# Optimization experiments

Measured on AMD Instinct MI355X. Metric: run time of the kernel, lower is better.

## Reference

```python
import jax, jax.numpy as jnp
import numpy as np

H = 1024      # hidden_size
NH = 16       # num_heads
HD = H // NH  # head_dim
E = 4096      # expand_size
EPS = 1e-5


def layernorm(x, w, b):
    mu = jnp.mean(x, axis=-1, keepdims=True)
    var = jnp.mean(jnp.square(x - mu), axis=-1, keepdims=True)
    return (x - mu) * jax.lax.rsqrt(var + EPS) * w + b


def setup_inputs() -> dict:
    key = jax.random.key(0)
    ks = jax.random.split(key, 8)
    s = 1.0 / np.sqrt(H)
    return {
        "x": jax.random.normal(ks[0], (4, 2048, H), dtype=jnp.float32),
        "ln1_w": jnp.ones((H,), jnp.float32),
        "ln1_b": jnp.zeros((H,), jnp.float32),
        "Wqkv": jax.random.normal(ks[1], (H, 3 * H), dtype=jnp.float32) * s,
        "bqkv": jnp.zeros((3 * H,), jnp.float32),
        "Wo": jax.random.normal(ks[2], (H, H), dtype=jnp.float32) * s,
        "bo": jnp.zeros((H,), jnp.float32),
        "ln2_w": jnp.ones((H,), jnp.float32),
        "ln2_b": jnp.zeros((H,), jnp.float32),
        "fc1_w": jax.random.normal(ks[3], (H, E), dtype=jnp.float32) * s,
        "fc1_b": jnp.zeros((E,), jnp.float32),
        "fc2_w": jax.random.normal(ks[4], (E, H), dtype=jnp.float32) * (1.0 / np.sqrt(E)),
        "fc2_b": jnp.zeros((H,), jnp.float32),
    }


def reference(x, ln1_w, ln1_b, Wqkv, bqkv, Wo, bo, ln2_w, ln2_b, fc1_w, fc1_b, fc2_w, fc2_b):
    B, S, C = x.shape
    # --- attention sub-block (pre-norm) ---
    h = layernorm(x, ln1_w, ln1_b)
    qkv = h @ Wqkv + bqkv                             # [B,S,3C]
    qkv = qkv.reshape(B, S, 3, NH, HD)
    q, k, v = (jnp.moveaxis(qkv[:, :, i], 2, 1) for i in range(3))  # [B,NH,S,HD]
    attn = jnp.einsum("bhqd,bhkd->bhqk", q, k) / np.sqrt(HD)        # [B,NH,S,S]
    attn = jax.nn.softmax(attn, axis=-1)
    o = jnp.einsum("bhqk,bhkd->bhqd", attn, v)        # [B,NH,S,HD]
    o = jnp.moveaxis(o, 1, 2).reshape(B, S, C)
    x = x + o @ Wo + bo
    # --- FFN sub-block (pre-norm) ---
    h = layernorm(x, ln2_w, ln2_b)
    h = jax.nn.gelu(h @ fc1_w + fc1_b, approximate=False)
    return x + h @ fc2_w + fc2_b
```

## Files before the change

### kernel.cpp

```cpp
#include <hip/hip_runtime.h>
#include <hip/hip_bf16.h>
#include <math.h>

typedef __bf16 bf16_t;
typedef __bf16 bf16x4 __attribute__((ext_vector_type(4)));
typedef short  s16x8  __attribute__((ext_vector_type(8)));
typedef float  f32x4  __attribute__((ext_vector_type(4)));

#define DEVINL __device__ __forceinline__

DEVINL void gload_lds16(const void* g, void* l) {
  __builtin_amdgcn_global_load_lds(
      (const __attribute__((address_space(1))) unsigned int*)g,
      (__attribute__((address_space(3))) unsigned int*)l, 16, 0, 0);
}

DEVINL f32x4 mfma16(s16x8 a, s16x8 b, f32x4 c) {
  return __builtin_amdgcn_mfma_f32_16x16x32_bf16(a, b, c, 0, 0, 0);
}

__global__ __launch_bounds__(256) void tcast_kernel(const float* __restrict__ W,
                                                    bf16_t* __restrict__ WT,
                                                    int K, int N) {
  __shared__ float tile[32][33];
  const int n0 = blockIdx.x * 32, k0 = blockIdx.y * 32;
  const int tx = threadIdx.x, ty = threadIdx.y;
#pragma unroll
  for (int j = 0; j < 4; ++j)
    tile[ty + j * 8][tx] = W[(size_t)(k0 + ty + j * 8) * N + (n0 + tx)];
  __syncthreads();
#pragma unroll
  for (int j = 0; j < 4; ++j)
    WT[(size_t)(n0 + ty + j * 8) * K + (k0 + tx)] = (bf16_t)tile[tx][ty + j * 8];
}

__global__ __launch_bounds__(256) void ln_kernel(const float* __restrict__ x,
                                                 const float* __restrict__ w,
                                                 const float* __restrict__ b,
                                                 bf16_t* __restrict__ out) {
  const int row = blockIdx.x, tid = threadIdx.x;
  const float4 v = ((const float4*)(x + (size_t)row * 1024))[tid];
  float s  = v.x + v.y + v.z + v.w;
  float s2 = v.x * v.x + v.y * v.y + v.z * v.z + v.w * v.w;
#pragma unroll
  for (int off = 32; off > 0; off >>= 1) {
    s  += __shfl_down(s, off);
    s2 += __shfl_down(s2, off);
  }
  __shared__ float red[8];
  const int wave = tid >> 6, lane = tid & 63;
  if (lane == 0) { red[wave] = s; red[4 + wave] = s2; }
  __syncthreads();
  s  = red[0] + red[1] + red[2] + red[3];
  s2 = red[4] + red[5] + red[6] + red[7];
  const float mu = s * (1.0f / 1024.0f);
  const float rs = rsqrtf(s2 * (1.0f / 1024.0f) - mu * mu + 1e-5f);
  const float4 wv = ((const float4*)w)[tid];
  const float4 bv = ((const float4*)b)[tid];
  bf16x4 o;
  o[0] = (bf16_t)((v.x - mu) * rs * wv.x + bv.x);
  o[1] = (bf16_t)((v.y - mu) * rs * wv.y + bv.y);
  o[2] = (bf16_t)((v.z - mu) * rs * wv.z + bv.z);
  o[3] = (bf16_t)((v.w - mu) * rs * wv.w + bv.w);
  ((bf16x4*)(out + (size_t)row * 1024))[tid] = o;
}

template <int EPI>
__global__ __launch_bounds__(256, 4) void gemm128b(const bf16_t* __restrict__ A,
                                                   const bf16_t* __restrict__ BT,
                                                   const float* __restrict__ bias,
                                                   const float* __restrict__ resid,
                                                   void* __restrict__ out,
                                                   void* __restrict__ out2,
                                                   int M, int N, int K) {
  __shared__ __align__(16) bf16_t sA[128 * 64];
  __shared__ __align__(16) bf16_t sB[128 * 64];
  const int tid = threadIdx.x;
  const int lane = tid & 63, wave = tid >> 6;
  const int wr = wave >> 1, wc = wave & 1;
  const int g = lane >> 4, lr = lane & 15;

  const int bid = blockIdx.x;
  const int cpx = gridDim.x >> 3;
  const int gid = (bid & 7) * cpx + (bid >> 3);
  const int m0 = (gid & 63) * 128, n0 = (gid >> 6) * 128;
  const bf16_t* Ab = A + (size_t)m0 * K;
  const bf16_t* Bb = BT + (size_t)n0 * K;

  f32x4 acc[4][4] = {};

  for (int kt = 0; kt < K; kt += 64) {
    __syncthreads();
#pragma unroll
    for (int q = 0; q < 4; ++q) {
      const int c = q * 256 + tid;
      const int r = c >> 3;
      const int j = (c & 7) ^ (r & 7);
      const size_t doff = (size_t)(q * 256 + wave * 64) * 8;
      gload_lds16(Ab + (size_t)r * K + kt + j * 8, sA + doff);
      gload_lds16(Bb + (size_t)r * K + kt + j * 8, sB + doff);
    }
    __syncthreads();
#pragma unroll
    for (int ks = 0; ks < 2; ++ks) {
      s16x8 af[4], bfr[4];
#pragma unroll
      for (int m = 0; m < 4; ++m) {
        const int r = wr * 64 + m * 16 + lr;
        af[m] = *(const s16x8*)&sA[r * 64 + (((ks << 2) + g) ^ (r & 7)) * 8];
      }
#pragma unroll
      for (int n = 0; n < 4; ++n) {
        const int r = wc * 64 + n * 16 + lr;
        bfr[n] = *(const s16x8*)&sB[r * 64 + (((ks << 2) + g) ^ (r & 7)) * 8];
      }
#pragma unroll
      for (int m = 0; m < 4; ++m)
#pragma unroll
        for (int n = 0; n < 4; ++n)
          acc[m][n] = mfma16(af[m], bfr[n], acc[m][n]);
    }
  }

#pragma unroll
  for (int m = 0; m < 4; ++m)
#pragma unroll
    for (int n = 0; n < 4; ++n) {
      const int col = n0 + wc * 64 + n * 16 + lr;
      const float bv = bias[col];
      const int rrow0 = m0 + wr * 64 + m * 16 + g * 4;
      if (EPI == 3 && col >= 2048) {
        const int col2 = col - 2048;
        bf16x4 pk;
#pragma unroll
        for (int i = 0; i < 4; ++i) pk[i] = (bf16_t)(acc[m][n][i] + bv);
        const size_t didx =
            ((((size_t)(rrow0 >> 11)) * 16 + (col2 >> 6)) * 64 + (col2 & 63)) * 2048 +
            (rrow0 & 2047);
        *(bf16x4*)&((bf16_t*)out2)[didx] = pk;
      } else {
#pragma unroll
        for (int i = 0; i < 4; ++i) {
          const int rrow = rrow0 + i;
          float v = acc[m][n][i] + bv;
          if (EPI == 1) {
            const size_t idx = (size_t)rrow * N + col;
            v += resid[idx];
            ((float*)out)[idx] = v;
          } else if (EPI == 2) {
            v = 0.5f * v * (1.0f + erff(v * 0.70710678118f));
            ((bf16_t*)out)[(size_t)rrow * N + col] = (bf16_t)v;
          } else if (EPI == 3) {
            ((bf16_t*)out)[(size_t)rrow * 2048 + col] = (bf16_t)v;
          } else {
            ((bf16_t*)out)[(size_t)rrow * N + col] = (bf16_t)v;
          }
        }
      }
    }
}

__global__ __launch_bounds__(256) void flash_attn2(const bf16_t* __restrict__ qk,
                                                   const bf16_t* __restrict__ vt,
                                                   bf16_t* __restrict__ O) {
  const int S = 2048;
  const int qt = blockIdx.x;
  const int bh = blockIdx.y;
  const int h = bh & 15;
  const size_t rowbase = (size_t)(bh >> 4) * S;
  const int tid = threadIdx.x, lane = tid & 63, wave = tid >> 6;
  const int g = lane >> 4, lr = lane & 15;
  const int q0w = qt * 64 + wave * 16;

  __shared__ __align__(16) bf16_t sK[64 * 64];
  __shared__ __align__(16) bf16_t sVT[64 * 64];
  __shared__ __align__(16) bf16_t sP[4][16 * 72];

  const bf16_t* vtb = vt + (size_t)bh * 64 * 2048;

  s16x8 aq[2];
  {
    const bf16_t* qrow = qk + (rowbase + q0w + lr) * 2048 + h * 64;
    aq[0] = *(const s16x8*)(qrow + g * 8);
    aq[1] = *(const s16x8*)(qrow + 32 + g * 8);
  }

  f32x4 oa[4] = {};
  float mrun = -1e30f, lrun = 0.0f;

  for (int kv0 = 0; kv0 < S; kv0 += 64) {
    __syncthreads();
#pragma unroll
    for (int p = 0; p < 2; ++p) {
      const int c = p * 256 + wave * 64 + lane;
      const int r = c >> 3;
      const int pb = (c & 7) ^ (r & 7);
      char* dK = (char*)sK + (size_t)(p * 256 + wave * 64) * 16;
      char* dV = (char*)sVT + (size_t)(p * 256 + wave * 64) * 16;
      gload_lds16(qk + (rowbase + kv0 + r) * 2048 + 1024 + h * 64 + pb * 8, dK);
      gload_lds16(vtb + (size_t)r * 2048 + kv0 + pb * 8, dV);
    }
    __syncthreads();

    f32x4 sc[4] = {};
#pragma unroll
    for (int st = 0; st < 2; ++st)
#pragma unroll
      for (int fr = 0; fr < 4; ++fr) {
        const int pb = (g + 4 * st) ^ (lr & 7);
        const s16x8 ak = *(const s16x8*)&sK[(fr * 16 + lr) * 64 + pb * 8];
        sc[fr] = mfma16(ak, aq[st], sc[fr]);
      }

    float rmax = -1e30f;
#pragma unroll
    for (int fr = 0; fr < 4; ++fr)
#pragma unroll
      for (int i = 0; i < 4; ++i) rmax = fmaxf(rmax, sc[fr][i]);
    rmax = fmaxf(rmax, __shfl_xor(rmax, 16));
    rmax = fmaxf(rmax, __shfl_xor(rmax, 32));
    const float mnew = fmaxf(mrun, rmax * 0.125f);
    const float alpha = __expf(mrun - mnew);
    mrun = mnew;
    float rsum = 0.0f;
#pragma unroll
    for (int fr = 0; fr < 4; ++fr)
#pragma unroll
      for (int i = 0; i < 4; ++i) {
        const float pp = __expf(sc[fr][i] * 0.125f - mnew);
        sc[fr][i] = pp;
        rsum += pp;
      }
    rsum += __shfl_xor(rsum, 16);
    rsum += __shfl_xor(rsum, 32);
    lrun = lrun * alpha + rsum;
#pragma unroll
    for (int f2 = 0; f2 < 4; ++f2)
#pragma unroll
      for (int i = 0; i < 4; ++i) oa[f2][i] *= alpha;

#pragma unroll
    for (int fr = 0; fr < 4; ++fr) {
      bf16x4 pk;
#pragma unroll
      for (int i = 0; i < 4; ++i) pk[i] = (bf16_t)sc[fr][i];
      *(bf16x4*)&sP[wave][lr * 72 + fr * 16 + 4 * g] = pk;
    }

#pragma unroll
    for (int st = 0; st < 2; ++st) {
      const s16x8 pa = *(const s16x8*)&sP[wave][lr * 72 + st * 32 + g * 8];
#pragma unroll
      for (int f2 = 0; f2 < 4; ++f2) {
        const int pb = (g + 4 * st) ^ (lr & 7);
        const s16x8 va = *(const s16x8*)&sVT[(f2 * 16 + lr) * 64 + pb * 8];
        oa[f2] = mfma16(va, pa, oa[f2]);
      }
    }
  }

  const float rl = 1.0f / lrun;
#pragma unroll
  for (int f2 = 0; f2 < 4; ++f2) {
    bf16x4 ov;
#pragma unroll
    for (int i = 0; i < 4; ++i) ov[i] = (bf16_t)(oa[f2][i] * rl);
    *(bf16x4*)&O[(rowbase + q0w + lr) * 1024 + h * 64 + f2 * 16 + 4 * g] = ov;
  }
}

extern "C" void kernel_launch(void* const* d_in, const int* in_sizes, int n_in,
                              void* d_out, int out_size, void* d_ws, size_t ws_size,
                              hipStream_t stream) {
  const float* x    = (const float*)d_in[0];
  const float* ln1w = (const float*)d_in[1];
  const float* ln1b = (const float*)d_in[2];
  const float* Wqkv = (const float*)d_in[3];
  const float* bqkv = (const float*)d_in[4];
  const float* Wo   = (const float*)d_in[5];
  const float* bo   = (const float*)d_in[6];
  const float* ln2w = (const float*)d_in[7];
  const float* ln2b = (const float*)d_in[8];
  const float* fc1w = (const float*)d_in[9];
  const float* fc1b = (const float*)d_in[10];
  const float* fc2w = (const float*)d_in[11];
  const float* fc2b = (const float*)d_in[12];

  const int M = 8192;

  char* ws = (char*)d_ws;
  size_t off = 0;
  auto alloc = [&](size_t bytes) {
    char* p = ws + off;
    off += (bytes + 255) & ~(size_t)255;
    return p;
  };
  bf16_t* WqkvT = (bf16_t*)alloc((size_t)3072 * 1024 * 2);
  bf16_t* WoT   = (bf16_t*)alloc((size_t)1024 * 1024 * 2);
  bf16_t* fc1T  = (bf16_t*)alloc((size_t)4096 * 1024 * 2);
  bf16_t* fc2T  = (bf16_t*)alloc((size_t)1024 * 4096 * 2);
  bf16_t* h1    = (bf16_t*)alloc((size_t)M * 1024 * 2);
  bf16_t* qkQK  = (bf16_t*)alloc((size_t)M * 2048 * 2);
  bf16_t* vTg   = (bf16_t*)alloc((size_t)M * 1024 * 2);
  bf16_t* attnO = (bf16_t*)alloc((size_t)M * 1024 * 2);
  float*  x2    = (float*)alloc((size_t)M * 1024 * 4);
  bf16_t* h2   = h1;
  bf16_t* gbuf = qkQK;
  if (off > ws_size) return;

  const dim3 tb(32, 8);
  tcast_kernel<<<dim3(96, 32), tb, 0, stream>>>(Wqkv, WqkvT, 1024, 3072);
  tcast_kernel<<<dim3(32, 32), tb, 0, stream>>>(Wo, WoT, 1024, 1024);
  tcast_kernel<<<dim3(128, 32), tb, 0, stream>>>(fc1w, fc1T, 1024, 4096);
  tcast_kernel<<<dim3(32, 128), tb, 0, stream>>>(fc2w, fc2T, 4096, 1024);

  ln_kernel<<<M, 256, 0, stream>>>(x, ln1w, ln1b, h1);

  gemm128b<3><<<dim3(1536), 256, 0, stream>>>(h1, WqkvT, bqkv, nullptr, qkQK, vTg, M, 3072, 1024);

  flash_attn2<<<dim3(32, 64), 256, 0, stream>>>(qkQK, vTg, attnO);

  gemm128b<1><<<dim3(512), 256, 0, stream>>>(attnO, WoT, bo, x, x2, nullptr, M, 1024, 1024);

  ln_kernel<<<M, 256, 0, stream>>>(x2, ln2w, ln2b, h2);

  gemm128b<2><<<dim3(2048), 256, 0, stream>>>(h2, fc1T, fc1b, nullptr, gbuf, nullptr, M, 4096, 1024);

  gemm128b<1><<<dim3(512), 256, 0, stream>>>(gbuf, fc2T, fc2b, x2, (float*)d_out, nullptr, M, 1024, 4096);
}
```

Measured before the change: 449.0 us.

## Process 32 query rows per wave in flash attention with lazy rescaling

Each wave now handles two 16-row query tiles (128 queries per block, half the blocks), so every K/V tile loaded into LDS is reused across twice as many queries. The softmax moves to exp2 with a folded scale constant and skips the running-max rescale unless the new max exceeds the old by more than 8 (log2 units). The P staging buffer uses an XOR-style rotated layout without padding, and s_setprio brackets the MFMA sections. The cost is more registers per thread and fewer blocks in flight, which may lower occupancy.

Result: slower. 471.6 us (+5.0%).

```diff
diff --git a/kernel.cpp b/kernel.cpp
--- a/kernel.cpp
+++ b/kernel.cpp
@@ -160,7 +160,7 @@
     }
 }
 
-__global__ __launch_bounds__(256) void flash_attn2(const bf16_t* __restrict__ qk,
+__global__ __launch_bounds__(256) void flash_attn3(const bf16_t* __restrict__ qk,
                                                    const bf16_t* __restrict__ vt,
                                                    bf16_t* __restrict__ O) {
   const int S = 2048;
@@ -170,23 +170,26 @@
   const size_t rowbase = (size_t)(bh >> 4) * S;
   const int tid = threadIdx.x, lane = tid & 63, wave = tid >> 6;
   const int g = lane >> 4, lr = lane & 15;
-  const int q0w = qt * 64 + wave * 16;
+  const int q0w = qt * 128 + wave * 32;
+  const float c2 = 0.18033688f;
 
   __shared__ __align__(16) bf16_t sK[64 * 64];
   __shared__ __align__(16) bf16_t sVT[64 * 64];
-  __shared__ __align__(16) bf16_t sP[4][16 * 72];
+  __shared__ __align__(16) bf16_t sP[4][16 * 64];
 
   const bf16_t* vtb = vt + (size_t)bh * 64 * 2048;
 
-  s16x8 aq[2];
-  {
-    const bf16_t* qrow = qk + (rowbase + q0w + lr) * 2048 + h * 64;
-    aq[0] = *(const s16x8*)(qrow + g * 8);
-    aq[1] = *(const s16x8*)(qrow + 32 + g * 8);
-  }
-
-  f32x4 oa[4] = {};
-  float mrun = -1e30f, lrun = 0.0f;
+  s16x8 aq[2][2];
+#pragma unroll
+  for (int hf = 0; hf < 2; ++hf) {
+    const bf16_t* qrow = qk + (rowbase + q0w + hf * 16 + lr) * 2048 + h * 64;
+    aq[hf][0] = *(const s16x8*)(qrow + g * 8);
+    aq[hf][1] = *(const s16x8*)(qrow + 32 + g * 8);
+  }
+
+  f32x4 oa[2][4] = {};
+  float m2[2] = {-1e30f, -1e30f};
+  float lrun[2] = {0.0f, 0.0f};
 
   for (int kv0 = 0; kv0 < S; kv0 += 64) {
     __syncthreads();
@@ -202,70 +205,87 @@
     }
     __syncthreads();
 
-    f32x4 sc[4] = {};
-#pragma unroll
-    for (int st = 0; st < 2; ++st)
+#pragma unroll
+    for (int hf = 0; hf < 2; ++hf) {
+      f32x4 sc[4] = {};
+      __builtin_amdgcn_s_setprio(1);
+#pragma unroll
+      for (int st = 0; st < 2; ++st)
+#pragma unroll
+        for (int fr = 0; fr < 4; ++fr) {
+          const int pb = (g + 4 * st) ^ (lr & 7);
+          const s16x8 ak = *(const s16x8*)&sK[(fr * 16 + lr) * 64 + pb * 8];
+          sc[fr] = mfma16(ak, aq[hf][st], sc[fr]);
+        }
+      __builtin_amdgcn_s_setprio(0);
+
+      float rmax = fmaxf(fmaxf(sc[0][0], sc[0][1]), fmaxf(sc[0][2], sc[0][3]));
+#pragma unroll
+      for (int fr = 1; fr < 4; ++fr)
+#pragma unroll
+        for (int i = 0; i < 4; ++i) rmax = fmaxf(rmax, sc[fr][i]);
+      rmax = fmaxf(rmax, __shfl_xor(rmax, 16));
+      rmax = fmaxf(rmax, __shfl_xor(rmax, 32));
+      const float pm2 = rmax * c2;
+      if (!__all(pm2 <= m2[hf] + 8.0f)) {
+        const float mn = fmaxf(m2[hf], pm2);
+        const float alpha = exp2f(m2[hf] - mn);
+        m2[hf] = mn;
+        lrun[hf] *= alpha;
+#pragma unroll
+        for (int f2 = 0; f2 < 4; ++f2)
+#pragma unroll
+          for (int i = 0; i < 4; ++i) oa[hf][f2][i] *= alpha;
+      }
+      const float mm = m2[hf];
+      float rsum = 0.0f;
+#pragma unroll
+      for (int fr = 0; fr < 4; ++fr)
+#pragma unroll
+        for (int i = 0; i < 4; ++i) {
+          const float pp = exp2f(fmaf(sc[fr][i], c2, -mm));
+          sc[fr][i] = pp;
+          rsum += pp;
+        }
+      rsum += __shfl_xor(rsum, 16);
+      rsum += __shfl_xor(rsum, 32);
+      lrun[hf] += rsum;
+
 #pragma unroll
       for (int fr = 0; fr < 4; ++fr) {
-        const int pb = (g + 4 * st) ^ (lr & 7);
-        const s16x8 ak = *(const s16x8*)&sK[(fr * 16 + lr) * 64 + pb * 8];
-        sc[fr] = mfma16(ak, aq[st], sc[fr]);
-      }
-
-    float rmax = -1e30f;
-#pragma unroll
-    for (int fr = 0; fr < 4; ++fr)
-#pragma unroll
-      for (int i = 0; i < 4; ++i) rmax = fmaxf(rmax, sc[fr][i]);
-    rmax = fmaxf(rmax, __shfl_xor(rmax, 16));
-    rmax = fmaxf(rmax, __shfl_xor(rmax, 32));
-    const float mnew = fmaxf(mrun, rmax * 0.125f);
-    const float alpha = __expf(mrun - mnew);
-    mrun = mnew;
-    float rsum = 0.0f;
-#pragma unroll
-    for (int fr = 0; fr < 4; ++fr)
-#pragma unroll
-      for (int i = 0; i < 4; ++i) {
-        const float pp = __expf(sc[fr][i] * 0.125f - mnew);
-        sc[fr][i] = pp;
-        rsum += pp;
-      }
-    rsum += __shfl_xor(rsum, 16);
-    rsum += __shfl_xor(rsum, 32);
-    lrun = lrun * alpha + rsum;
-#pragma unroll
-    for (int f2 = 0; f2 < 4; ++f2)
-#pragma unroll
-      for (int i = 0; i < 4; ++i) oa[f2][i] *= alpha;
-
-#pragma unroll
-    for (int fr = 0; fr < 4; ++fr) {
-      bf16x4 pk;
-#pragma unroll
-      for (int i = 0; i < 4; ++i) pk[i] = (bf16_t)sc[fr][i];
-      *(bf16x4*)&sP[wave][lr * 72 + fr * 16 + 4 * g] = pk;
-    }
-
-#pragma unroll
-    for (int st = 0; st < 2; ++st) {
-      const s16x8 pa = *(const s16x8*)&sP[wave][lr * 72 + st * 32 + g * 8];
-#pragma unroll
-      for (int f2 = 0; f2 < 4; ++f2) {
-        const int pb = (g + 4 * st) ^ (lr & 7);
-        const s16x8 va = *(const s16x8*)&sVT[(f2 * 16 + lr) * 64 + pb * 8];
-        oa[f2] = mfma16(va, pa, oa[f2]);
-      }
-    }
-  }
-
-  const float rl = 1.0f / lrun;
-#pragma unroll
-  for (int f2 = 0; f2 < 4; ++f2) {
-    bf16x4 ov;
-#pragma unroll
-    for (int i = 0; i < 4; ++i) ov[i] = (bf16_t)(oa[f2][i] * rl);
-    *(bf16x4*)&O[(rowbase + q0w + lr) * 1024 + h * 64 + f2 * 16 + 4 * g] = ov;
+        bf16x4 pk;
+#pragma unroll
+        for (int i = 0; i < 4; ++i) pk[i] = (bf16_t)sc[fr][i];
+        const int c = fr * 2 + (g >> 1);
+        *(bf16x4*)&sP[wave][lr * 64 + ((c + lr) & 7) * 8 + 4 * (g & 1)] = pk;
+      }
+
+      __builtin_amdgcn_s_setprio(1);
+#pragma unroll
+      for (int st = 0; st < 2; ++st) {
+        const int pc = st * 4 + g;
+        const s16x8 pa = *(const s16x8*)&sP[wave][lr * 64 + ((pc + lr) & 7) * 8];
+#pragma unroll
+        for (int f2 = 0; f2 < 4; ++f2) {
+          const int pb = (g + 4 * st) ^ (lr & 7);
+          const s16x8 va = *(const s16x8*)&sVT[(f2 * 16 + lr) * 64 + pb * 8];
+          oa[hf][f2] = mfma16(va, pa, oa[hf][f2]);
+        }
+      }
+      __builtin_amdgcn_s_setprio(0);
+    }
+  }
+
+#pragma unroll
+  for (int hf = 0; hf < 2; ++hf) {
+    const float rl = 1.0f / lrun[hf];
+#pragma unroll
+    for (int f2 = 0; f2 < 4; ++f2) {
+      bf16x4 ov;
+#pragma unroll
+      for (int i = 0; i < 4; ++i) ov[i] = (bf16_t)(oa[hf][f2][i] * rl);
+      *(bf16x4*)&O[(rowbase + q0w + hf * 16 + lr) * 1024 + h * 64 + f2 * 16 + 4 * g] = ov;
+    }
   }
 }
 
@@ -318,7 +338,7 @@
 
   gemm128b<3><<<dim3(1536), 256, 0, stream>>>(h1, WqkvT, bqkv, nullptr, qkQK, vTg, M, 3072, 1024);
 
-  flash_attn2<<<dim3(32, 64), 256, 0, stream>>>(qkQK, vTg, attnO);
+  flash_attn3<<<dim3(16, 64), 256, 0, stream>>>(qkQK, vTg, attnO);
 
   gemm128b<1><<<dim3(512), 256, 0, stream>>>(attnO, WoT, bo, x, x2, nullptr, M, 1024, 1024);
 
```

## Double-buffer K/V tiles and add lazy rescaling with exp2 in flash attention

Applied to the files above, without the earlier changes.

The attention kernel now double-buffers the K and V^T tiles in LDS, so the next tile is issued into the other buffer while the current one is computed, and each iteration needs one barrier instead of two. Softmax uses exp2 with a pre-folded log2e/sqrt(d) scale, and the output/denominator rescale is skipped unless some row's max grows by more than 8 in log2 space. The P scratch buffer drops its padding in favour of an XOR-like rotated layout, and s_setprio is raised around the MFMA sections. In exchange it doubles K/V LDS use, which may lower occupancy. The lazy rescale lets exponentials reach up to 2^8 before renormalisation, which shifts bf16 rounding of P slightly.

Result: slower. 463.4 us (+3.2%).

```diff
diff --git a/kernel.cpp b/kernel.cpp
--- a/kernel.cpp
+++ b/kernel.cpp
@@ -160,7 +160,7 @@
     }
 }
 
-__global__ __launch_bounds__(256) void flash_attn2(const bf16_t* __restrict__ qk,
+__global__ __launch_bounds__(256) void flash_attn4(const bf16_t* __restrict__ qk,
                                                    const bf16_t* __restrict__ vt,
                                                    bf16_t* __restrict__ O) {
   const int S = 2048;
@@ -171,12 +171,34 @@
   const int tid = threadIdx.x, lane = tid & 63, wave = tid >> 6;
   const int g = lane >> 4, lr = lane & 15;
   const int q0w = qt * 64 + wave * 16;
-
-  __shared__ __align__(16) bf16_t sK[64 * 64];
-  __shared__ __align__(16) bf16_t sVT[64 * 64];
-  __shared__ __align__(16) bf16_t sP[4][16 * 72];
+  const float c2 = 0.18033688f;
+
+  __shared__ __align__(16) bf16_t sK[2][64 * 64];
+  __shared__ __align__(16) bf16_t sVT[2][64 * 64];
+  __shared__ __align__(16) bf16_t sP[4][16 * 64];
 
   const bf16_t* vtb = vt + (size_t)bh * 64 * 2048;
+
+  const bf16_t* kp[2];
+  const bf16_t* vp[2];
+  int ldsoff[2];
+#pragma unroll
+  for (int p = 0; p < 2; ++p) {
+    const int cp = p * 256 + wave * 64 + lane;
+    const int r = cp >> 3;
+    const int pb = (cp & 7) ^ (r & 7);
+    kp[p] = qk + (rowbase + r) * 2048 + 1024 + h * 64 + pb * 8;
+    vp[p] = vtb + (size_t)r * 2048 + pb * 8;
+    ldsoff[p] = (p * 256 + wave * 64) * 16;
+  }
+  auto stage = [&](int t, int buf) {
+    const int kvoff = t << 6;
+#pragma unroll
+    for (int p = 0; p < 2; ++p) {
+      gload_lds16(kp[p] + (size_t)kvoff * 2048, (char*)sK[buf] + ldsoff[p]);
+      gload_lds16(vp[p] + kvoff, (char*)sVT[buf] + ldsoff[p]);
+    }
+  };
 
   s16x8 aq[2];
   {
@@ -186,77 +208,80 @@
   }
 
   f32x4 oa[4] = {};
-  float mrun = -1e30f, lrun = 0.0f;
-
-  for (int kv0 = 0; kv0 < S; kv0 += 64) {
+  float m2 = -1e30f, lrun = 0.0f;
+
+  stage(0, 0);
+
+  for (int t = 0; t < 32; ++t) {
+    const int cur = t & 1;
     __syncthreads();
-#pragma unroll
-    for (int p = 0; p < 2; ++p) {
-      const int c = p * 256 + wave * 64 + lane;
-      const int r = c >> 3;
-      const int pb = (c & 7) ^ (r & 7);
-      char* dK = (char*)sK + (size_t)(p * 256 + wave * 64) * 16;
-      char* dV = (char*)sVT + (size_t)(p * 256 + wave * 64) * 16;
-      gload_lds16(qk + (rowbase + kv0 + r) * 2048 + 1024 + h * 64 + pb * 8, dK);
-      gload_lds16(vtb + (size_t)r * 2048 + kv0 + pb * 8, dV);
-    }
-    __syncthreads();
+    if (t + 1 < 32) stage(t + 1, cur ^ 1);
 
     f32x4 sc[4] = {};
+    __builtin_amdgcn_s_setprio(1);
 #pragma unroll
     for (int st = 0; st < 2; ++st)
 #pragma unroll
       for (int fr = 0; fr < 4; ++fr) {
         const int pb = (g + 4 * st) ^ (lr & 7);
-        const s16x8 ak = *(const s16x8*)&sK[(fr * 16 + lr) * 64 + pb * 8];
+        const s16x8 ak = *(const s16x8*)&sK[cur][(fr * 16 + lr) * 64 + pb * 8];
         sc[fr] = mfma16(ak, aq[st], sc[fr]);
       }
-
-    float rmax = -1e30f;
-#pragma unroll
-    for (int fr = 0; fr < 4; ++fr)
+    __builtin_amdgcn_s_setprio(0);
+
+    float rmax = fmaxf(fmaxf(sc[0][0], sc[0][1]), fmaxf(sc[0][2], sc[0][3]));
+#pragma unroll
+    for (int fr = 1; fr < 4; ++fr)
 #pragma unroll
       for (int i = 0; i < 4; ++i) rmax = fmaxf(rmax, sc[fr][i]);
     rmax = fmaxf(rmax, __shfl_xor(rmax, 16));
     rmax = fmaxf(rmax, __shfl_xor(rmax, 32));
-    const float mnew = fmaxf(mrun, rmax * 0.125f);
-    const float alpha = __expf(mrun - mnew);
-    mrun = mnew;
+    const float pm2 = rmax * c2;
+    if (!__all(pm2 <= m2 + 8.0f)) {
+      const float mn = fmaxf(m2, pm2);
+      const float alpha = exp2f(m2 - mn);
+      m2 = mn;
+      lrun *= alpha;
+#pragma unroll
+      for (int f2 = 0; f2 < 4; ++f2)
+#pragma unroll
+        for (int i = 0; i < 4; ++i) oa[f2][i] *= alpha;
+    }
     float rsum = 0.0f;
 #pragma unroll
     for (int fr = 0; fr < 4; ++fr)
 #pragma unroll
       for (int i = 0; i < 4; ++i) {
-        const float pp = __expf(sc[fr][i] * 0.125f - mnew);
+        const float pp = exp2f(fmaf(sc[fr][i], c2, -m2));
         sc[fr][i] = pp;
         rsum += pp;
       }
     rsum += __shfl_xor(rsum, 16);
     rsum += __shfl_xor(rsum, 32);
-    lrun = lrun * alpha + rsum;
-#pragma unroll
-    for (int f2 = 0; f2 < 4; ++f2)
-#pragma unroll
-      for (int i = 0; i < 4; ++i) oa[f2][i] *= alpha;
+    lrun += rsum;
 
 #pragma unroll
     for (int fr = 0; fr < 4; ++fr) {
       bf16x4 pk;
 #pragma unroll
       for (int i = 0; i < 4; ++i) pk[i] = (bf16_t)sc[fr][i];
-      *(bf16x4*)&sP[wave][lr * 72 + fr * 16 + 4 * g] = pk;
-    }
-
+      const int c = fr * 2 + (g >> 1);
+      *(bf16x4*)&sP[wave][lr * 64 + ((c + lr) & 7) * 8 + 4 * (g & 1)] = pk;
+    }
+
+    __builtin_amdgcn_s_setprio(1);
 #pragma unroll
     for (int st = 0; st < 2; ++st) {
-      const s16x8 pa = *(const s16x8*)&sP[wave][lr * 72 + st * 32 + g * 8];
+      const int pc = st * 4 + g;
+      const s16x8 pa = *(const s16x8*)&sP[wave][lr * 64 + ((pc + lr) & 7) * 8];
 #pragma unroll
       for (int f2 = 0; f2 < 4; ++f2) {
         const int pb = (g + 4 * st) ^ (lr & 7);
-        const s16x8 va = *(const s16x8*)&sVT[(f2 * 16 + lr) * 64 + pb * 8];
+        const s16x8 va = *(const s16x8*)&sVT[cur][(f2 * 16 + lr) * 64 + pb * 8];
         oa[f2] = mfma16(va, pa, oa[f2]);
       }
     }
+    __builtin_amdgcn_s_setprio(0);
   }
 
   const float rl = 1.0f / lrun;
@@ -318,7 +343,7 @@
 
   gemm128b<3><<<dim3(1536), 256, 0, stream>>>(h1, WqkvT, bqkv, nullptr, qkQK, vTg, M, 3072, 1024);
 
-  flash_attn2<<<dim3(32, 64), 256, 0, stream>>>(qkQK, vTg, attnO);
+  flash_attn4<<<dim3(32, 64), 256, 0, stream>>>(qkQK, vTg, attnO);
 
   gemm128b<1><<<dim3(512), 256, 0, stream>>>(attnO, WoT, bo, x, x2, nullptr, M, 1024, 1024);
 
```
